# Kernel tuning notes

Hardware: AMD Instinct MI355X
Metric: run time of the kernel (lower is better)

## Reference

```python
import jax, jax.numpy as jnp
import numpy as np

B, L, H = 2, 2048, 1536
I, N, R, K = 3072, 16, 96, 4


def setup_inputs() -> dict:
    key = jax.random.key(0)
    ks = jax.random.split(key, 10)
    rn = lambda k, shape, s: jax.random.normal(k, shape, jnp.float32) * s
    return {
        "hidden_states": rn(ks[0], (B, L, H), 1.0),
        "W_in": rn(ks[1], (2 * I, H), 0.02),
        "conv_w": rn(ks[2], (I, K), 0.1),
        "conv_b": rn(ks[3], (I,), 0.1),
        "W_x": rn(ks[4], (R + 2 * N, I), 0.02),
        "W_dt": rn(ks[5], (I, R), 0.02),
        "dt_bias": rn(ks[6], (I,), 0.1),
        # vLLM's weight loader stores A = -exp(A_log); replicate that here
        "A": -jnp.exp(rn(ks[7], (I, N), 0.5)),
        "D": jnp.ones((I,), jnp.float32),
        "W_out": rn(ks[8], (H, I), 0.02),
    }


def reference(hidden_states, W_in, conv_w, conv_b, W_x, W_dt, dt_bias, A, D, W_out):
    b, l, _ = hidden_states.shape
    k = conv_w.shape[1]
    n = A.shape[1]
    r = W_dt.shape[1]

    # in_proj -> [B,L,2I], split into ssm input x and gate
    proj = jnp.einsum("blh,eh->ble", hidden_states, W_in)
    x, gate = jnp.split(proj, 2, axis=-1)  # each [B,L,I]

    # causal depthwise conv1d over L (pad K-1 on the left) + SiLU
    xp = jnp.pad(x, ((0, 0), (k - 1, 0), (0, 0)))
    conv = sum(xp[:, j : j + l, :] * conv_w[:, j] for j in range(k)) + conv_b
    x = jax.nn.silu(conv)  # [B,L,I]

    # x_proj -> dt (rank R), B, C (each N)
    ssm_p = jnp.einsum("bli,pi->blp", x, W_x)
    dt_in, Bm, Cm = jnp.split(ssm_p, [r, r + n], axis=-1)

    # dt_proj (skip_bias_add) then softplus(dt + bias) inside the scan math
    dt = jnp.einsum("blr,ir->bli", dt_in, W_dt)
    delta = jax.nn.softplus(dt + dt_bias)  # [B,L,I]

    # selective scan: s_t = exp(delta_t * A) * s_{t-1} + delta_t * x_t * B_t
    def step(state, inp):
        d_t, u_t, B_t, C_t = inp  # [B,I], [B,I], [B,N], [B,N]
        dA = jnp.exp(d_t[..., None] * A)  # [B,I,N]
        state = state * dA + (d_t * u_t)[..., None] * B_t[:, None, :]
        y = jnp.einsum("bin,bn->bi", state, C_t)
        return state, y

    init = jnp.zeros((b, x.shape[-1], n), jnp.float32)
    _, ys = jax.lax.scan(
        step,
        init,
        (
            delta.transpose(1, 0, 2),
            x.transpose(1, 0, 2),
            Bm.transpose(1, 0, 2),
            Cm.transpose(1, 0, 2),
        ),
    )
    y = ys.transpose(1, 0, 2) + x * D  # skip connection via D
    y = y * jax.nn.silu(gate)

    # out_proj -> [B,L,H]
    return jnp.einsum("bli,hi->blh", y, W_out)
```

## Files before the change

### kernel.cpp

```cpp
#include <hip/hip_runtime.h>

typedef __attribute__((ext_vector_type(8))) short bf16x8;
typedef __attribute__((ext_vector_type(4))) float f32x4;

#define CCH 32
#define TCH 64

__device__ __forceinline__ unsigned short f2b(float f) {
    unsigned u = __float_as_uint(f);
    return (unsigned short)((u + 0x7fffu + ((u >> 16) & 1u)) >> 16);
}
__device__ __forceinline__ float b2f(unsigned short h) {
    return __uint_as_float(((unsigned)h) << 16);
}
__device__ __forceinline__ float softplus_f(float z) {
    return (z > 15.f) ? z : __logf(1.f + __expf(z));
}
__device__ __forceinline__ float silu_f(float g) {
    return g / (1.f + __expf(-g));
}

__device__ __forceinline__ void gload16(const unsigned short* g, unsigned short* l) {
    __builtin_amdgcn_global_load_lds(
        (const __attribute__((address_space(1))) void*)g,
        (__attribute__((address_space(3))) void*)l, 16, 0, 0);
}

__global__ __launch_bounds__(256)
void cast_all(const float* __restrict__ h, const float* __restrict__ win,
              const float* __restrict__ wx, const float* __restrict__ wdt,
              const float* __restrict__ wout,
              unsigned short* __restrict__ dh, unsigned short* __restrict__ dwin,
              unsigned short* __restrict__ dwx, unsigned short* __restrict__ dwdt,
              unsigned short* __restrict__ dwout) {
    const int n0 = 1572864, n1 = n0 + 2359296, n2 = n1 + 98304,
              n3 = n2 + 73728, n4 = n3 + 1179648;
    int i = blockIdx.x * 256 + threadIdx.x;
    const float* s; unsigned short* d; int off;
    if (i < n0)      { s = h;    d = dh;    off = i; }
    else if (i < n1) { s = win;  d = dwin;  off = i - n0; }
    else if (i < n2) { s = wx;   d = dwx;   off = i - n1; }
    else if (i < n3) { s = wdt;  d = dwdt;  off = i - n2; }
    else if (i < n4) { s = wout; d = dwout; off = i - n3; }
    else return;
    float4 v = reinterpret_cast<const float4*>(s)[off];
    ushort4 o;
    o.x = f2b(v.x); o.y = f2b(v.y); o.z = f2b(v.z); o.w = f2b(v.w);
    reinterpret_cast<ushort4*>(d)[off] = o;
}

template <int OP>
__global__ __launch_bounds__(512)
void gemm256(const unsigned short* __restrict__ A, const unsigned short* __restrict__ W,
             void* __restrict__ Cout, int Kc, int lda, int ldw, int ldc,
             int ntx, int nty, int silu_col0, long long czs) {
    __shared__ __align__(16) unsigned short lds[65536];
    const int tid  = threadIdx.x;
    const int lane = tid & 63;
    const int wave = tid >> 6;
    const int wr   = wave >> 2;
    const int wc   = wave & 3;
    const int lr   = lane & 15;
    const int quad = lane >> 4;
    const int sw   = lr & 7;

    const int c = blockIdx.x & 7;
    const int j = blockIdx.x >> 3;
    int bm_t, bn_t;
    if ((ntx & 7) == 0) {
        const int cpx = ntx >> 3;
        bn_t = c * cpx + j % cpx;
        bm_t = j / cpx;
    } else {
        const int rpx = nty >> 3;
        bm_t = c * rpx + j % rpx;
        bn_t = j / rpx;
    }
    const int bm = bm_t * 256;
    const int bn = bn_t * 256;
    const int kz = blockIdx.z;
    A += (size_t)kz * Kc;
    W += (size_t)kz * Kc;

    const int rsub = wave * 8 + (lane >> 3);
    const int csw  = ((lane & 7) ^ ((lane >> 3) & 7)) * 8;
    const unsigned short* gA = A + (size_t)(bm + rsub) * lda + csw;
    const unsigned short* gB = W + (size_t)(bn + rsub) * ldw + csw;

#define STA(b, h, kt) do { \
        gload16(gA + (size_t)((h) * 128) * lda + (kt) * 64,      &lds[(b) * 16384 + (h) * 8192 + wave * 512]); \
        gload16(gA + (size_t)((h) * 128 + 64) * lda + (kt) * 64, &lds[(b) * 16384 + (h) * 8192 + 4096 + wave * 512]); \
    } while (0)
#define STB(b, h, kt) do { \
        gload16(gB + (size_t)((h) * 128) * ldw + (kt) * 64,      &lds[32768 + (b) * 16384 + (h) * 8192 + wave * 512]); \
        gload16(gB + (size_t)((h) * 128 + 64) * ldw + (kt) * 64, &lds[32768 + (b) * 16384 + (h) * 8192 + 4096 + wave * 512]); \
    } while (0)

#define LDA_F(b, mh, mi, kk) \
    (*reinterpret_cast<const bf16x8*>(&lds[(b) * 16384 + ((mh) * 128 + wr * 64 + (mi) * 16 + lr) * 64 + (((((kk) << 2) | quad)) ^ sw) * 8]))
#define LDB_F(b, nh, ni, kk) \
    (*reinterpret_cast<const bf16x8*>(&lds[32768 + (b) * 16384 + ((nh) * 128 + wc * 32 + (ni) * 16 + lr) * 64 + (((((kk) << 2) | quad)) ^ sw) * 8]))

#define RD_A(b, mh) do { \
        _Pragma("unroll") for (int mi = 0; mi < 4; ++mi) { \
            fa[mi][0] = LDA_F(b, mh, mi, 0); \
            fa[mi][1] = LDA_F(b, mh, mi, 1); } } while (0)
#define RD_B(b, nh, dst) do { \
        _Pragma("unroll") for (int ni = 0; ni < 2; ++ni) { \
            dst[ni][0] = LDB_F(b, nh, ni, 0); \
            dst[ni][1] = LDB_F(b, nh, ni, 1); } } while (0)

#define MFMA_Q(mh, nh, bb) do { \
        _Pragma("unroll") for (int mi = 0; mi < 4; ++mi) \
        _Pragma("unroll") for (int ni = 0; ni < 2; ++ni) { \
            acc[(mh) * 4 + mi][(nh) * 2 + ni] = __builtin_amdgcn_mfma_f32_16x16x32_bf16(fa[mi][0], bb[ni][0], acc[(mh) * 4 + mi][(nh) * 2 + ni], 0, 0, 0); \
            acc[(mh) * 4 + mi][(nh) * 2 + ni] = __builtin_amdgcn_mfma_f32_16x16x32_bf16(fa[mi][1], bb[ni][1], acc[(mh) * 4 + mi][(nh) * 2 + ni], 0, 0, 0); } } while (0)

#define MIDB  asm volatile("s_barrier" ::: "memory")
#define LGKM0 asm volatile("s_waitcnt lgkmcnt(0)" ::: "memory")
#define ENDB  asm volatile("s_barrier" ::: "memory")
#define ENDB_VM8 asm volatile("s_waitcnt vmcnt(8)\n\ts_barrier" ::: "memory")
#define ENDB_VM0 asm volatile("s_waitcnt vmcnt(0)\n\ts_barrier" ::: "memory")
#define PRIO1 __builtin_amdgcn_s_setprio(1)
#define PRIO0 __builtin_amdgcn_s_setprio(0)

    f32x4 acc[8][4];
    const f32x4 zero = {0.f, 0.f, 0.f, 0.f};
#pragma unroll
    for (int m = 0; m < 8; ++m)
#pragma unroll
        for (int n = 0; n < 4; ++n) acc[m][n] = zero;

    bf16x8 fa[4][2], fb0[2][2], fb1[2][2];

    const int nkt = Kc >> 6;
    const int NT2 = nkt >> 1;

    STA(0, 0, 0); STB(0, 0, 0); STA(0, 1, 0); STB(0, 1, 0);
    STA(1, 0, 1); STB(1, 0, 1); STA(1, 1, 1); STB(1, 1, 1);
    ENDB_VM8;

#pragma unroll 1
    for (int t = 0; t < NT2 - 1; ++t) {
        const int k2 = 2 * t + 2, k3 = 2 * t + 3;
        RD_A(0, 0); RD_B(0, 0, fb0);
        MIDB; LGKM0; PRIO1; MFMA_Q(0, 0, fb0); PRIO0; ENDB;
        RD_B(0, 1, fb1); STA(0, 0, k2); STB(0, 0, k2);
        MIDB; LGKM0; PRIO1; MFMA_Q(0, 1, fb1); PRIO0; ENDB;
        RD_A(0, 1); STB(0, 1, k2);
        MIDB; LGKM0; PRIO1; MFMA_Q(1, 0, fb0); PRIO0; ENDB;
        STA(0, 1, k2);
        MIDB; PRIO1; MFMA_Q(1, 1, fb1); PRIO0; ENDB_VM8;
        RD_A(1, 0); RD_B(1, 0, fb0);
        MIDB; LGKM0; PRIO1; MFMA_Q(0, 0, fb0); PRIO0; ENDB;
        RD_B(1, 1, fb1); STA(1, 0, k3); STB(1, 0, k3);
        MIDB; LGKM0; PRIO1; MFMA_Q(0, 1, fb1); PRIO0; ENDB;
        RD_A(1, 1); STB(1, 1, k3);
        MIDB; LGKM0; PRIO1; MFMA_Q(1, 0, fb0); PRIO0; ENDB;
        STA(1, 1, k3);
        MIDB; PRIO1; MFMA_Q(1, 1, fb1); PRIO0; ENDB_VM8;
    }
    {
        RD_A(0, 0); RD_B(0, 0, fb0);
        MIDB; LGKM0; PRIO1; MFMA_Q(0, 0, fb0); PRIO0; ENDB;
        RD_B(0, 1, fb1);
        MIDB; LGKM0; PRIO1; MFMA_Q(0, 1, fb1); PRIO0; ENDB;
        RD_A(0, 1);
        MIDB; LGKM0; PRIO1; MFMA_Q(1, 0, fb0); PRIO0; ENDB;
        MIDB; PRIO1; MFMA_Q(1, 1, fb1); PRIO0; ENDB_VM0;
        RD_A(1, 0); RD_B(1, 0, fb0);
        MIDB; LGKM0; PRIO1; MFMA_Q(0, 0, fb0); PRIO0; ENDB;
        RD_B(1, 1, fb1);
        MIDB; LGKM0; PRIO1; MFMA_Q(0, 1, fb1); PRIO0; ENDB;
        RD_A(1, 1);
        MIDB; LGKM0; PRIO1; MFMA_Q(1, 0, fb0); PRIO0; ENDB;
        MIDB; PRIO1; MFMA_Q(1, 1, fb1); PRIO0;
    }

#pragma unroll
    for (int m = 0; m < 8; ++m) {
        const int row0 = bm + (m >> 2) * 128 + wr * 64 + (m & 3) * 16 + quad * 4;
#pragma unroll
        for (int n = 0; n < 4; ++n) {
            const int col = bn + (n >> 1) * 128 + wc * 32 + (n & 1) * 16 + lr;
#pragma unroll
            for (int reg = 0; reg < 4; ++reg) {
                float v = acc[m][n][reg];
                if (OP == 0) {
                    float* Cf = (float*)Cout + (size_t)kz * czs;
                    Cf[(size_t)(row0 + reg) * ldc + col] = v;
                } else {
                    if (col >= silu_col0) v = silu_f(v);
                    ((unsigned short*)Cout)[(size_t)(row0 + reg) * ldc + col] = f2b(v);
                }
            }
        }
    }
#undef STA
#undef STB
#undef LDA_F
#undef LDB_F
#undef RD_A
#undef RD_B
#undef MFMA_Q
#undef MIDB
#undef LGKM0
#undef ENDB
#undef ENDB_VM8
#undef ENDB_VM0
#undef PRIO1
#undef PRIO0
}

template <int OP>
__global__ __launch_bounds__(256)
void gemm_mfma(const unsigned short* __restrict__ A, const unsigned short* __restrict__ W,
               void* __restrict__ Cout, int Kc, int lda, int ldw, int ldc,
               const float* __restrict__ bias, int silu_col0, long long czs) {
    __shared__ unsigned short As[3][4096];
    __shared__ unsigned short Bs[3][4096];
    const int tid = threadIdx.x;
    const int bm = blockIdx.y * 128;
    const int bn = blockIdx.x * 128;
    const int kz = blockIdx.z;
    A += (size_t)kz * Kc;
    W += (size_t)kz * Kc;
    const int lane = tid & 63;
    const int wave = tid >> 6;
    const int r_a = lane >> 2;
    const int k8 = (lane & 3) * 8;

    const unsigned short* gA0 = A + (size_t)(bm + wave * 16 + r_a) * lda + k8;
    const unsigned short* gA1 = A + (size_t)(bm + 64 + wave * 16 + r_a) * lda + k8;
    const unsigned short* gB0 = W + (size_t)(bn + wave * 16 + r_a) * ldw + k8;
    const unsigned short* gB1 = W + (size_t)(bn + 64 + wave * 16 + r_a) * ldw + k8;

    const int wm = (wave & 1) * 64;
    const int wn = (wave >> 1) * 64;
    const int lr = lane & 15;
    const int quad = lane >> 4;

    f32x4 acc[4][4];
    const f32x4 zero = {0.f, 0.f, 0.f, 0.f};
#pragma unroll
    for (int i = 0; i < 4; i++)
#pragma unroll
        for (int j = 0; j < 4; j++) acc[i][j] = zero;

#define STAGE(koff, j) do { \
        gload16(gA0 + (koff), As[j] + wave * 512); \
        gload16(gA1 + (koff), As[j] + (wave + 4) * 512); \
        gload16(gB0 + (koff), Bs[j] + wave * 512); \
        gload16(gB1 + (koff), Bs[j] + (wave + 4) * 512); \
    } while (0)

    const int niter = Kc >> 5;
    STAGE(0, 0);
    if (niter > 1) STAGE(32, 1);

    int ib = 0;
    for (int k = 0; k < niter; k++) {
        if (k + 1 < niter)
            asm volatile("s_waitcnt vmcnt(4)\n\ts_barrier" ::: "memory");
        else
            asm volatile("s_waitcnt vmcnt(0)\n\ts_barrier" ::: "memory");
        if (k + 2 < niter) {
            int is_ = ib + 2; if (is_ >= 3) is_ -= 3;
            STAGE((k + 2) << 5, is_);
        }
        const unsigned short* as = As[ib];
        const unsigned short* bs = Bs[ib];
        bf16x8 fa[4], fb[4];
#pragma unroll
        for (int mi = 0; mi < 4; mi++)
            fa[mi] = *reinterpret_cast<const bf16x8*>(as + (wm + mi * 16 + lr) * 32 + quad * 8);
#pragma unroll
        for (int ni = 0; ni < 4; ni++)
            fb[ni] = *reinterpret_cast<const bf16x8*>(bs + (wn + ni * 16 + lr) * 32 + quad * 8);
#pragma unroll
        for (int mi = 0; mi < 4; mi++)
#pragma unroll
            for (int ni = 0; ni < 4; ni++)
                acc[mi][ni] = __builtin_amdgcn_mfma_f32_16x16x32_bf16(fa[mi], fb[ni], acc[mi][ni], 0, 0, 0);
        ib = (ib == 2) ? 0 : ib + 1;
    }
#undef STAGE

#pragma unroll
    for (int mi = 0; mi < 4; mi++)
#pragma unroll
        for (int reg = 0; reg < 4; reg++) {
            int row = bm + wm + mi * 16 + quad * 4 + reg;
#pragma unroll
            for (int ni = 0; ni < 4; ni++) {
                int col = bn + wn + ni * 16 + lr;
                float v = acc[mi][ni][reg];
                if (OP == 0) {
                    float* Cf = (float*)Cout + (size_t)kz * czs;
                    Cf[(size_t)row * ldc + col] = v;
                } else if (OP == 2) {
                    if (col >= silu_col0) v = silu_f(v);
                    ((unsigned short*)Cout)[(size_t)row * ldc + col] = f2b(v);
                } else {
                    ((unsigned short*)Cout)[(size_t)row * ldc + col] = f2b(softplus_f(v + bias[col]));
                }
            }
        }
}

__global__ __launch_bounds__(256)
void reduce_out(const float* __restrict__ p, float* __restrict__ out, int n4) {
    int i = blockIdx.x * 256 + threadIdx.x;
    if (i >= n4) return;
    float4 a = reinterpret_cast<const float4*>(p)[i];
    float4 b = reinterpret_cast<const float4*>(p + (size_t)n4 * 4)[i];
    float4 o = {a.x + b.x, a.y + b.y, a.z + b.z, a.w + b.w};
    reinterpret_cast<float4*>(out)[i] = o;
}

__global__ __launch_bounds__(256)
void reduce_xpart(const float* __restrict__ xpart, float* __restrict__ ssmp,
                  unsigned short* __restrict__ dtin) {
    const int BL = 4096;
    int idx = blockIdx.x * 256 + threadIdx.x;
    int row = idx >> 5;
    int c4 = (idx & 31) * 4;
    float4 s = {0.f, 0.f, 0.f, 0.f};
#pragma unroll
    for (int z = 0; z < 8; z++) {
        float4 v = *reinterpret_cast<const float4*>(xpart + (size_t)z * BL * 128 + (size_t)row * 128 + c4);
        s.x += v.x; s.y += v.y; s.z += v.z; s.w += v.w;
    }
    *reinterpret_cast<float4*>(ssmp + (size_t)row * 128 + c4) = s;
    if (c4 < 96) {
        ushort4 o;
        o.x = f2b(s.x); o.y = f2b(s.y); o.z = f2b(s.z); o.w = f2b(s.w);
        *reinterpret_cast<ushort4*>(dtin + (size_t)row * 96 + c4) = o;
    }
}

__global__ __launch_bounds__(256)
void conv_silu8(const unsigned short* __restrict__ projbf, const float* __restrict__ cw,
                const float* __restrict__ cb, unsigned short* __restrict__ xc) {
    const int I = 3072, L = 2048, LD = 6144;
    int idx = blockIdx.x * 256 + threadIdx.x;
    int i8 = (idx % (I / 8)) * 8;
    int bl = idx / (I / 8);
    int l = bl & (L - 1);
    float s[8];
    {
        float4 b0 = *reinterpret_cast<const float4*>(cb + i8);
        float4 b1 = *reinterpret_cast<const float4*>(cb + i8 + 4);
        s[0]=b0.x; s[1]=b0.y; s[2]=b0.z; s[3]=b0.w; s[4]=b1.x; s[5]=b1.y; s[6]=b1.z; s[7]=b1.w;
    }
    float w[8][4];
#pragma unroll
    for (int c = 0; c < 8; c++) {
        float4 wr = *reinterpret_cast<const float4*>(cw + (i8 + c) * 4);
        w[c][0]=wr.x; w[c][1]=wr.y; w[c][2]=wr.z; w[c][3]=wr.w;
    }
#pragma unroll
    for (int j = 0; j < 4; j++) {
        if (l + j - 3 >= 0) {
            uint4 r = *reinterpret_cast<const uint4*>(projbf + (size_t)(bl + j - 3) * LD + i8);
            float xv[8];
            xv[0]=b2f((unsigned short)(r.x & 0xffff)); xv[1]=b2f((unsigned short)(r.x >> 16));
            xv[2]=b2f((unsigned short)(r.y & 0xffff)); xv[3]=b2f((unsigned short)(r.y >> 16));
            xv[4]=b2f((unsigned short)(r.z & 0xffff)); xv[5]=b2f((unsigned short)(r.z >> 16));
            xv[6]=b2f((unsigned short)(r.w & 0xffff)); xv[7]=b2f((unsigned short)(r.w >> 16));
#pragma unroll
            for (int c = 0; c < 8; c++) s[c] = fmaf(xv[c], w[c][j], s[c]);
        }
    }
    unsigned short o[8];
#pragma unroll
    for (int c = 0; c < 8; c++) o[c] = f2b(silu_f(s[c]));
    uint4 packed;
    packed.x = (unsigned)o[0] | ((unsigned)o[1] << 16);
    packed.y = (unsigned)o[2] | ((unsigned)o[3] << 16);
    packed.z = (unsigned)o[4] | ((unsigned)o[5] << 16);
    packed.w = (unsigned)o[6] | ((unsigned)o[7] << 16);
    *reinterpret_cast<uint4*>(xc + (size_t)bl * I + i8) = packed;
}

__global__ __launch_bounds__(256)
void scan_passA(const unsigned short* __restrict__ delta_bf, const unsigned short* __restrict__ xc,
                const float* __restrict__ ssmp, const float* __restrict__ Aw,
                float* __restrict__ S_local, float* __restrict__ sumDelta) {
    const int I = 3072, L = 2048;
    __shared__ float bc[TCH][32];
    int g = blockIdx.x * 256 + threadIdx.x;
    int i = g % I;
    int bcid = g / I;
    int c = bcid % CCH;
    int b = bcid / CCH;
    size_t rowbase = (size_t)b * L + (size_t)c * TCH;
    for (int e = threadIdx.x; e < TCH * 8; e += 256) {
        int t = e >> 3, q = e & 7;
        float4 v = *reinterpret_cast<const float4*>(ssmp + (rowbase + t) * 128 + 96 + q * 4);
        *reinterpret_cast<float4*>(&bc[t][q * 4]) = v;
    }
    __syncthreads();

    float Arow[16];
#pragma unroll
    for (int n = 0; n < 16; n++) Arow[n] = Aw[i * 16 + n];
    float st[16];
#pragma unroll
    for (int n = 0; n < 16; n++) st[n] = 0.f;
    float sumD = 0.f;

    size_t rowI = rowbase * I + i;
    for (int t = 0; t < TCH; t++) {
        float delta = b2f(delta_bf[rowI]);
        float du = delta * b2f(xc[rowI]);
        sumD += delta;
        float4 b0 = *reinterpret_cast<const float4*>(&bc[t][0]);
        float4 b1 = *reinterpret_cast<const float4*>(&bc[t][4]);
        float4 b2 = *reinterpret_cast<const float4*>(&bc[t][8]);
        float4 b3 = *reinterpret_cast<const float4*>(&bc[t][12]);
        const float bv[16] = {b0.x,b0.y,b0.z,b0.w, b1.x,b1.y,b1.z,b1.w,
                              b2.x,b2.y,b2.z,b2.w, b3.x,b3.y,b3.z,b3.w};
#pragma unroll
        for (int n = 0; n < 16; n++)
            st[n] = fmaf(st[n], __expf(delta * Arow[n]), du * bv[n]);
        rowI += I;
    }
    size_t obase = (size_t)bcid * 16 * I + i;
#pragma unroll
    for (int n = 0; n < 16; n++) S_local[obase + (size_t)n * I] = st[n];
    sumDelta[(size_t)bcid * I + i] = sumD;
}

__global__ __launch_bounds__(256)
void scan_passB(const float* __restrict__ S_local, const float* __restrict__ sumDelta,
                const float* __restrict__ Aw, float* __restrict__ state_in) {
    const int I = 3072;
    int g = blockIdx.x * 256 + threadIdx.x;
    int i = g % I;
    int bn = g / I;
    int n = bn & 15;
    int b = bn >> 4;
    float a = Aw[i * 16 + n];
    float state = 0.f;
    for (int c = 0; c < CCH; c++) {
        int bcid = b * CCH + c;
        size_t idx = ((size_t)bcid * 16 + n) * I + i;
        state_in[idx] = state;
        state = fmaf(state, __expf(a * sumDelta[(size_t)bcid * I + i]), S_local[idx]);
    }
}

__global__ __launch_bounds__(256)
void scan_passC(const unsigned short* __restrict__ projbf,
                const unsigned short* __restrict__ xc,
                const float* __restrict__ ssmp, const unsigned short* __restrict__ delta_bf,
                const float* __restrict__ Aw, const float* __restrict__ Dw,
                const float* __restrict__ state_in, unsigned short* __restrict__ ybf) {
    const int I = 3072, L = 2048, LD = 6144;
    __shared__ float bc[TCH][32];
    int g = blockIdx.x * 256 + threadIdx.x;
    int i = g % I;
    int bcid = g / I;
    int c = bcid % CCH;
    int b = bcid / CCH;
    size_t rowbase = (size_t)b * L + (size_t)c * TCH;
    for (int e = threadIdx.x; e < TCH * 8; e += 256) {
        int t = e >> 3, q = e & 7;
        float4 v = *reinterpret_cast<const float4*>(ssmp + (rowbase + t) * 128 + 96 + q * 4);
        *reinterpret_cast<float4*>(&bc[t][q * 4]) = v;
    }
    __syncthreads();

    float Arow[16];
#pragma unroll
    for (int n = 0; n < 16; n++) Arow[n] = Aw[i * 16 + n];
    float Dv = Dw[i];
    float st[16];
    size_t sbase = (size_t)bcid * 16 * I + i;
#pragma unroll
    for (int n = 0; n < 16; n++) st[n] = state_in[sbase + (size_t)n * I];

    size_t rowI = rowbase * I + i;
    size_t rowG = rowbase * LD + I + i;
    for (int t = 0; t < TCH; t++) {
        float delta = b2f(delta_bf[rowI]);
        float u = b2f(xc[rowI]);
        float du = delta * u;
        float4 b0 = *reinterpret_cast<const float4*>(&bc[t][0]);
        float4 b1 = *reinterpret_cast<const float4*>(&bc[t][4]);
        float4 b2 = *reinterpret_cast<const float4*>(&bc[t][8]);
        float4 b3 = *reinterpret_cast<const float4*>(&bc[t][12]);
        float4 c0 = *reinterpret_cast<const float4*>(&bc[t][16]);
        float4 c1 = *reinterpret_cast<const float4*>(&bc[t][20]);
        float4 c2 = *reinterpret_cast<const float4*>(&bc[t][24]);
        float4 c3 = *reinterpret_cast<const float4*>(&bc[t][28]);
        const float bv[16] = {b0.x,b0.y,b0.z,b0.w, b1.x,b1.y,b1.z,b1.w,
                              b2.x,b2.y,b2.z,b2.w, b3.x,b3.y,b3.z,b3.w};
        const float cv[16] = {c0.x,c0.y,c0.z,c0.w, c1.x,c1.y,c1.z,c1.w,
                              c2.x,c2.y,c2.z,c2.w, c3.x,c3.y,c3.z,c3.w};
        float y = 0.f;
#pragma unroll
        for (int n = 0; n < 16; n++) {
            st[n] = fmaf(st[n], __expf(delta * Arow[n]), du * bv[n]);
            y = fmaf(st[n], cv[n], y);
        }
        y = fmaf(u, Dv, y);
        y *= b2f(projbf[rowG]);
        ybf[rowI] = f2b(y);
        rowI += I;
        rowG += LD;
    }
}

extern "C" void kernel_launch(void* const* d_in, const int* in_sizes, int n_in,
                              void* d_out, int out_size, void* d_ws, size_t ws_size,
                              hipStream_t stream) {
    const float* hidden  = (const float*)d_in[0];
    const float* W_in    = (const float*)d_in[1];
    const float* conv_w  = (const float*)d_in[2];
    const float* conv_b  = (const float*)d_in[3];
    const float* W_x     = (const float*)d_in[4];
    const float* W_dt    = (const float*)d_in[5];
    const float* dt_bias = (const float*)d_in[6];
    const float* Aw      = (const float*)d_in[7];
    const float* Dw      = (const float*)d_in[8];
    const float* W_out   = (const float*)d_in[9];
    float* out = (float*)d_out;

    constexpr int Bsz = 2, L = 2048, H = 1536, I = 3072, R = 96;
    constexpr int BL = Bsz * L;
    constexpr int TwoI = 2 * I;

    char* base = (char*)d_ws;
    unsigned short* proj_bf  = (unsigned short*)base; base += (size_t)BL * TwoI * 2;
    unsigned short* delta_bf = (unsigned short*)base; base += (size_t)BL * I * 2;
    unsigned short* xc_bf    = (unsigned short*)base; base += (size_t)BL * I * 2;
    unsigned short* y_bf     = (unsigned short*)base; base += (size_t)BL * I * 2;
    float* ssmp              = (float*)base;          base += (size_t)BL * 128 * 4;
    float* xpart             = (float*)base;          base += (size_t)8 * BL * 128 * 4;
    unsigned short* dtin_bf  = (unsigned short*)base; base += (size_t)BL * R * 2;
    unsigned short* wx_bf    = (unsigned short*)base; base += (size_t)128 * I * 2;
    unsigned short* wdt_bf   = (unsigned short*)base; base += (size_t)I * R * 2;
    unsigned short* wout_bf  = (unsigned short*)base; base += (size_t)H * I * 2;
    unsigned short* h_bf     = (unsigned short*)base; base += (size_t)BL * H * 2;
    unsigned short* win_bf   = (unsigned short*)base; base += (size_t)TwoI * H * 2;
    float* S_local  = (float*)h_bf;
    float* sumDelta = S_local + (size_t)Bsz * CCH * 16 * I;
    float* state_in = sumDelta + (size_t)Bsz * CCH * I;
    float* opart = (float*)proj_bf;

    dim3 blk(256);

    cast_all<<<(5283840 + 255) / 256, blk, 0, stream>>>(
        hidden, W_in, W_x, W_dt, W_out, h_bf, win_bf, wx_bf, wdt_bf, wout_bf);

    gemm256<2><<<dim3(24 * 16, 1, 1), dim3(512), 0, stream>>>(
        h_bf, win_bf, proj_bf, H, H, H, TwoI,  TwoI / 256,  BL / 256,
         I, 0);

    conv_silu8<<<BL * I / 8 / 256, blk, 0, stream>>>(proj_bf, conv_w, conv_b, xc_bf);

    gemm_mfma<0><<<dim3(1, BL / 128, 8), blk, 0, stream>>>(
        xc_bf, wx_bf, xpart, I / 8, I, I, 128, nullptr, 0, (long long)BL * 128);
    reduce_xpart<<<BL * 32 / 256, blk, 0, stream>>>(xpart, ssmp, dtin_bf);

    gemm_mfma<3><<<dim3(I / 128, BL / 128, 1), blk, 0, stream>>>(
        dtin_bf, wdt_bf, delta_bf, R, R, R, I, dt_bias, 0, 0);

    scan_passA<<<Bsz * I * CCH / 256, blk, 0, stream>>>(
        delta_bf, xc_bf, ssmp, Aw, S_local, sumDelta);
    scan_passB<<<Bsz * 16 * I / 256, blk, 0, stream>>>(
        S_local, sumDelta, Aw, state_in);
    scan_passC<<<Bsz * I * CCH / 256, blk, 0, stream>>>(
        proj_bf, xc_bf, ssmp, delta_bf, Aw, Dw, state_in, y_bf);

    gemm256<0><<<dim3(6 * 16, 1, 2), dim3(512), 0, stream>>>(
        y_bf, wout_bf, opart, I / 2, I, I, H,  H / 256,  BL / 256,
        0, (long long)BL * H);
    reduce_out<<<BL * H / 4 / 256, blk, 0, stream>>>(opart, out, BL * H / 4);
}
```

Baseline: 473.5 us.

## Restructure 256x256 GEMM main loop with double-buffered register fragments and finer vmcnt waits

```diff
diff --git a/kernel.cpp b/kernel.cpp
--- a/kernel.cpp
+++ b/kernel.cpp
@@ -87,13 +87,13 @@
     const unsigned short* gA = A + (size_t)(bm + rsub) * lda + csw;
     const unsigned short* gB = W + (size_t)(bn + rsub) * ldw + csw;
 
-#define STA(b, h, kt) do { \
-        gload16(gA + (size_t)((h) * 128) * lda + (kt) * 64,      &lds[(b) * 16384 + (h) * 8192 + wave * 512]); \
-        gload16(gA + (size_t)((h) * 128 + 64) * lda + (kt) * 64, &lds[(b) * 16384 + (h) * 8192 + 4096 + wave * 512]); \
+#define STA(b, h, koff) do { \
+        gload16(gA + (size_t)((h) * 128) * lda + (koff),      &lds[(b) * 16384 + (h) * 8192 + wave * 512]); \
+        gload16(gA + (size_t)((h) * 128 + 64) * lda + (koff), &lds[(b) * 16384 + (h) * 8192 + 4096 + wave * 512]); \
     } while (0)
-#define STB(b, h, kt) do { \
-        gload16(gB + (size_t)((h) * 128) * ldw + (kt) * 64,      &lds[32768 + (b) * 16384 + (h) * 8192 + wave * 512]); \
-        gload16(gB + (size_t)((h) * 128 + 64) * ldw + (kt) * 64, &lds[32768 + (b) * 16384 + (h) * 8192 + 4096 + wave * 512]); \
+#define STB(b, h, koff) do { \
+        gload16(gB + (size_t)((h) * 128) * ldw + (koff),      &lds[32768 + (b) * 16384 + (h) * 8192 + wave * 512]); \
+        gload16(gB + (size_t)((h) * 128 + 64) * ldw + (koff), &lds[32768 + (b) * 16384 + (h) * 8192 + 4096 + wave * 512]); \
     } while (0)
 
 #define LDA_F(b, mh, mi, kk) \
@@ -101,26 +101,26 @@
 #define LDB_F(b, nh, ni, kk) \
     (*reinterpret_cast<const bf16x8*>(&lds[32768 + (b) * 16384 + ((nh) * 128 + wc * 32 + (ni) * 16 + lr) * 64 + (((((kk) << 2) | quad)) ^ sw) * 8]))
 
-#define RD_A(b, mh) do { \
+#define RD_A(b, mh, DST) do { \
         _Pragma("unroll") for (int mi = 0; mi < 4; ++mi) { \
-            fa[mi][0] = LDA_F(b, mh, mi, 0); \
-            fa[mi][1] = LDA_F(b, mh, mi, 1); } } while (0)
-#define RD_B(b, nh, dst) do { \
+            DST[mi][0] = LDA_F(b, mh, mi, 0); \
+            DST[mi][1] = LDA_F(b, mh, mi, 1); } } while (0)
+#define RD_B(b, nh, DST) do { \
         _Pragma("unroll") for (int ni = 0; ni < 2; ++ni) { \
-            dst[ni][0] = LDB_F(b, nh, ni, 0); \
-            dst[ni][1] = LDB_F(b, nh, ni, 1); } } while (0)
-
-#define MFMA_Q(mh, nh, bb) do { \
+            DST[ni][0] = LDB_F(b, nh, ni, 0); \
+            DST[ni][1] = LDB_F(b, nh, ni, 1); } } while (0)
+
+#define MFMA_Q(mh, nh, FA, FB) do { \
         _Pragma("unroll") for (int mi = 0; mi < 4; ++mi) \
         _Pragma("unroll") for (int ni = 0; ni < 2; ++ni) { \
-            acc[(mh) * 4 + mi][(nh) * 2 + ni] = __builtin_amdgcn_mfma_f32_16x16x32_bf16(fa[mi][0], bb[ni][0], acc[(mh) * 4 + mi][(nh) * 2 + ni], 0, 0, 0); \
-            acc[(mh) * 4 + mi][(nh) * 2 + ni] = __builtin_amdgcn_mfma_f32_16x16x32_bf16(fa[mi][1], bb[ni][1], acc[(mh) * 4 + mi][(nh) * 2 + ni], 0, 0, 0); } } while (0)
+            acc[(mh) * 4 + mi][(nh) * 2 + ni] = __builtin_amdgcn_mfma_f32_16x16x32_bf16(FA[mi][0], FB[ni][0], acc[(mh) * 4 + mi][(nh) * 2 + ni], 0, 0, 0); \
+            acc[(mh) * 4 + mi][(nh) * 2 + ni] = __builtin_amdgcn_mfma_f32_16x16x32_bf16(FA[mi][1], FB[ni][1], acc[(mh) * 4 + mi][(nh) * 2 + ni], 0, 0, 0); } } while (0)
 
 #define MIDB  asm volatile("s_barrier" ::: "memory")
-#define LGKM0 asm volatile("s_waitcnt lgkmcnt(0)" ::: "memory")
-#define ENDB  asm volatile("s_barrier" ::: "memory")
-#define ENDB_VM8 asm volatile("s_waitcnt vmcnt(8)\n\ts_barrier" ::: "memory")
-#define ENDB_VM0 asm volatile("s_waitcnt vmcnt(0)\n\ts_barrier" ::: "memory")
+#define VM6B  asm volatile("s_waitcnt vmcnt(6)\n\ts_barrier" ::: "memory")
+#define VM4B  asm volatile("s_waitcnt vmcnt(4)\n\ts_barrier" ::: "memory")
+#define VM2B  asm volatile("s_waitcnt vmcnt(2)\n\ts_barrier" ::: "memory")
+#define VM0B  asm volatile("s_waitcnt vmcnt(0)\n\ts_barrier" ::: "memory")
 #define PRIO1 __builtin_amdgcn_s_setprio(1)
 #define PRIO0 __builtin_amdgcn_s_setprio(0)
 
@@ -131,50 +131,52 @@
 #pragma unroll
         for (int n = 0; n < 4; ++n) acc[m][n] = zero;
 
-    bf16x8 fa[4][2], fb0[2][2], fb1[2][2];
+    bf16x8 faA[4][2], faB[4][2], fbA[2][2], fbB[2][2];
 
     const int nkt = Kc >> 6;
-    const int NT2 = nkt >> 1;
 
     STA(0, 0, 0); STB(0, 0, 0); STA(0, 1, 0); STB(0, 1, 0);
-    STA(1, 0, 1); STB(1, 0, 1); STA(1, 1, 1); STB(1, 1, 1);
-    ENDB_VM8;
+    STB(1, 0, 64); STA(1, 0, 64);
+    VM6B;
+    RD_A(0, 0, faA); RD_B(0, 0, fbA);
 
 #pragma unroll 1
-    for (int t = 0; t < NT2 - 1; ++t) {
-        const int k2 = 2 * t + 2, k3 = 2 * t + 3;
-        RD_A(0, 0); RD_B(0, 0, fb0);
-        MIDB; LGKM0; PRIO1; MFMA_Q(0, 0, fb0); PRIO0; ENDB;
-        RD_B(0, 1, fb1); STA(0, 0, k2); STB(0, 0, k2);
-        MIDB; LGKM0; PRIO1; MFMA_Q(0, 1, fb1); PRIO0; ENDB;
-        RD_A(0, 1); STB(0, 1, k2);
-        MIDB; LGKM0; PRIO1; MFMA_Q(1, 0, fb0); PRIO0; ENDB;
-        STA(0, 1, k2);
-        MIDB; PRIO1; MFMA_Q(1, 1, fb1); PRIO0; ENDB_VM8;
-        RD_A(1, 0); RD_B(1, 0, fb0);
-        MIDB; LGKM0; PRIO1; MFMA_Q(0, 0, fb0); PRIO0; ENDB;
-        RD_B(1, 1, fb1); STA(1, 0, k3); STB(1, 0, k3);
-        MIDB; LGKM0; PRIO1; MFMA_Q(0, 1, fb1); PRIO0; ENDB;
-        RD_A(1, 1); STB(1, 1, k3);
-        MIDB; LGKM0; PRIO1; MFMA_Q(1, 0, fb0); PRIO0; ENDB;
-        STA(1, 1, k3);
-        MIDB; PRIO1; MFMA_Q(1, 1, fb1); PRIO0; ENDB_VM8;
+    for (int i = 0; i < (nkt - 2) / 2; ++i) {
+        RD_A(0, 1, faB); STA(1, 1, 64);
+        MIDB; PRIO1; MFMA_Q(0, 0, faA, fbA); PRIO0; VM6B;
+        RD_B(0, 1, fbB); STB(1, 1, 64);
+        MIDB; PRIO1; MFMA_Q(1, 0, faB, fbA); PRIO0; VM6B;
+        RD_B(1, 0, fbA); STB(0, 0, 128);
+        MIDB; PRIO1; MFMA_Q(0, 1, faA, fbB); PRIO0; VM6B;
+        RD_A(1, 0, faA); STA(0, 0, 128);
+        MIDB; PRIO1; MFMA_Q(1, 1, faB, fbB); PRIO0; VM6B;
+        RD_A(1, 1, faB); STA(0, 1, 128);
+        MIDB; PRIO1; MFMA_Q(0, 0, faA, fbA); PRIO0; VM6B;
+        RD_B(1, 1, fbB); STB(0, 1, 128);
+        MIDB; PRIO1; MFMA_Q(1, 0, faB, fbA); PRIO0; VM6B;
+        RD_B(0, 0, fbA); STB(1, 0, 192);
+        MIDB; PRIO1; MFMA_Q(0, 1, faA, fbB); PRIO0; VM6B;
+        RD_A(0, 0, faA); STA(1, 0, 192);
+        MIDB; PRIO1; MFMA_Q(1, 1, faB, fbB); PRIO0; VM6B;
+        gA += 128; gB += 128;
     }
     {
-        RD_A(0, 0); RD_B(0, 0, fb0);
-        MIDB; LGKM0; PRIO1; MFMA_Q(0, 0, fb0); PRIO0; ENDB;
-        RD_B(0, 1, fb1);
-        MIDB; LGKM0; PRIO1; MFMA_Q(0, 1, fb1); PRIO0; ENDB;
-        RD_A(0, 1);
-        MIDB; LGKM0; PRIO1; MFMA_Q(1, 0, fb0); PRIO0; ENDB;
-        MIDB; PRIO1; MFMA_Q(1, 1, fb1); PRIO0; ENDB_VM0;
-        RD_A(1, 0); RD_B(1, 0, fb0);
-        MIDB; LGKM0; PRIO1; MFMA_Q(0, 0, fb0); PRIO0; ENDB;
-        RD_B(1, 1, fb1);
-        MIDB; LGKM0; PRIO1; MFMA_Q(0, 1, fb1); PRIO0; ENDB;
-        RD_A(1, 1);
-        MIDB; LGKM0; PRIO1; MFMA_Q(1, 0, fb0); PRIO0; ENDB;
-        MIDB; PRIO1; MFMA_Q(1, 1, fb1); PRIO0;
+        RD_A(0, 1, faB); STA(1, 1, 64);
+        MIDB; PRIO1; MFMA_Q(0, 0, faA, fbA); PRIO0; VM6B;
+        RD_B(0, 1, fbB); STB(1, 1, 64);
+        MIDB; PRIO1; MFMA_Q(1, 0, faB, fbA); PRIO0; VM6B;
+        RD_B(1, 0, fbA);
+        MIDB; PRIO1; MFMA_Q(0, 1, faA, fbB); PRIO0; VM4B;
+        RD_A(1, 0, faA);
+        MIDB; PRIO1; MFMA_Q(1, 1, faB, fbB); PRIO0; VM2B;
+        RD_A(1, 1, faB);
+        MIDB; PRIO1; MFMA_Q(0, 0, faA, fbA); PRIO0; VM0B;
+        RD_B(1, 1, fbB);
+        PRIO1;
+        MFMA_Q(1, 0, faB, fbA);
+        MFMA_Q(0, 1, faA, fbB);
+        MFMA_Q(1, 1, faB, fbB);
+        PRIO0;
     }
 
 #pragma unroll
@@ -204,10 +206,10 @@
 #undef RD_B
 #undef MFMA_Q
 #undef MIDB
-#undef LGKM0
-#undef ENDB
-#undef ENDB_VM8
-#undef ENDB_VM0
+#undef VM6B
+#undef VM4B
+#undef VM2B
+#undef VM0B
 #undef PRIO1
 #undef PRIO0
 }
```

Result: slower. 655.9 us (+38.5%).
